# Performance work log

Measured on AMD Instinct MI355X. Metric: run time of the kernel, lower is better.

Reference implementation:

```python
import jax, jax.numpy as jnp
import numpy as np

B, T, C = 4, 2048, 1024
H = 16
HD = C // H  # 64


def setup_inputs() -> dict:
    key = jax.random.key(0)
    ks = jax.random.split(key, 4)
    x = jax.random.normal(ks[0], (B, T, C), dtype=jnp.float32)
    # c_attn: Linear(C, 3C, bias=False)  (qkv_bias=False)
    w_attn = jax.random.normal(ks[1], (C, 3 * C), dtype=jnp.float32) / np.sqrt(C)
    # c_proj: Linear(C, C) with bias (nn.Linear default)
    w_proj = jax.random.normal(ks[2], (C, C), dtype=jnp.float32) / np.sqrt(C)
    b_proj = jax.random.normal(ks[3], (C,), dtype=jnp.float32) * 0.01
    return {"x": x, "w_attn": w_attn, "w_proj": w_proj, "b_proj": b_proj}


def reference(x, w_attn, w_proj, b_proj):
    b, t, c = x.shape
    qkv = x @ w_attn  # [B,T,3C]
    q, k, v = jnp.split(qkv, 3, axis=-1)
    # [B,H,T,HD]
    q = q.reshape(b, t, H, HD).transpose(0, 2, 1, 3)
    k = k.reshape(b, t, H, HD).transpose(0, 2, 1, 3)
    v = v.reshape(b, t, H, HD).transpose(0, 2, 1, 3)
    scale = 1.0 / np.sqrt(HD)
    attn = jnp.einsum('bhqd,bhkd->bhqk', q, k) * scale  # [B,H,T,T]
    causal = jnp.tril(jnp.ones((t, t), dtype=bool))
    attn = jnp.where(causal, attn, -jnp.inf)
    attn = jax.nn.softmax(attn, axis=-1)
    out = jnp.einsum('bhqk,bhkd->bhqd', attn, v)  # [B,H,T,HD]
    out = out.transpose(0, 2, 1, 3).reshape(b, t, c)
    return out @ w_proj + b_proj
```

## Files before the change

### kernel.cpp

```cpp
#include <hip/hip_runtime.h>

#define BB 4
#define TT 2048
#define CC 1024
#define C3 3072
#define HH 16
#define HD 64
#define BT 8192

#define TS 40
#define TSZ (64 * TS)

typedef __bf16 bf16x8 __attribute__((ext_vector_type(8)));
typedef float floatx4 __attribute__((ext_vector_type(4)));
typedef unsigned short u16;

__device__ __forceinline__ u16 f2bf(float f) {
  union { float f; unsigned u; } a; a.f = f;
  return (u16)((a.u + 0x7fffu + ((a.u >> 16) & 1u)) >> 16);
}
__device__ __forceinline__ bf16x8 ld8(const u16* p) { return *(const bf16x8*)p; }
__device__ __forceinline__ floatx4 mfma16(bf16x8 a, bf16x8 b, floatx4 c) {
  return __builtin_amdgcn_mfma_f32_16x16x32_bf16(a, b, c, 0, 0, 0);
}

__global__ __launch_bounds__(256) void tobf16_kernel(const float4* __restrict__ src,
                                                     ushort4* __restrict__ dst, int n4) {
  int i = blockIdx.x * 256 + threadIdx.x;
  if (i >= n4) return;
  float4 v = src[i];
  ushort4 o; o.x = f2bf(v.x); o.y = f2bf(v.y); o.z = f2bf(v.z); o.w = f2bf(v.w);
  dst[i] = o;
}

__global__ __launch_bounds__(256) void transpose_bf16_kernel(const float* __restrict__ src,
                                                             u16* __restrict__ dst,
                                                             int K, int N) {
  __shared__ float s[64][65];
  const int t = threadIdx.x;
  const int r = t >> 4;
  const int c = (t & 15) * 4;
  const int k0 = blockIdx.y * 64, n0 = blockIdx.x * 64;
#pragma unroll
  for (int i = 0; i < 4; ++i) {
    float4 v = *(const float4*)&src[(size_t)(k0 + r + i * 16) * N + n0 + c];
    s[r + i * 16][c + 0] = v.x; s[r + i * 16][c + 1] = v.y;
    s[r + i * 16][c + 2] = v.z; s[r + i * 16][c + 3] = v.w;
  }
  __syncthreads();
#pragma unroll
  for (int i = 0; i < 4; ++i) {
    const int nn = r + i * 16;
    ushort4 o;
    o.x = f2bf(s[c + 0][nn]); o.y = f2bf(s[c + 1][nn]);
    o.z = f2bf(s[c + 2][nn]); o.w = f2bf(s[c + 3][nn]);
    *(ushort4*)&dst[(size_t)(n0 + nn) * K + k0 + c] = o;
  }
}

template<int MODE>
__global__ __launch_bounds__(256) void gemm_kernel(
    const u16* __restrict__ A, const u16* __restrict__ B,
    const float* __restrict__ bias, float* __restrict__ outf,
    u16* __restrict__ qk, u16* __restrict__ vT,
    int M, int N, int K) {
  __shared__ u16 smem[2][2][2 * TSZ];

  const int t = threadIdx.x;
  const int w = t >> 6, lane = t & 63, lr = lane & 15, qd = lane >> 4;
  const int wm = w >> 1, wn = w & 1;
  const int m0 = blockIdx.y * 128, n0 = blockIdx.x * 128;

  const int sr = t >> 2;
  const int sc = (t & 3) * 8;
  const int so = sr * TS + sc;
  const u16* Ag = A + (size_t)(m0 + sr) * K + sc;
  const u16* Bg = B + (size_t)(n0 + sr) * K + sc;

  floatx4 acc[4][4] = {};

  uint4 rA0, rA1, rB0, rB1;
  rA0 = *(const uint4*)(Ag);
  rA1 = *(const uint4*)(Ag + (size_t)64 * K);
  rB0 = *(const uint4*)(Bg);
  rB1 = *(const uint4*)(Bg + (size_t)64 * K);

  for (int k0 = 0; k0 < K; k0 += 32) {
    const int p = (k0 >> 5) & 1;
    u16* sA = &smem[p][0][0];
    u16* sB = &smem[p][1][0];
    *(uint4*)&sA[so]       = rA0;
    *(uint4*)&sA[TSZ + so] = rA1;
    *(uint4*)&sB[so]       = rB0;
    *(uint4*)&sB[TSZ + so] = rB1;
    __syncthreads();
    if (k0 + 32 < K) {
      rA0 = *(const uint4*)(Ag + k0 + 32);
      rA1 = *(const uint4*)(Ag + (size_t)64 * K + k0 + 32);
      rB0 = *(const uint4*)(Bg + k0 + 32);
      rB1 = *(const uint4*)(Bg + (size_t)64 * K + k0 + 32);
    }

    bf16x8 af[4], bf[4];
#pragma unroll
    for (int mj = 0; mj < 4; ++mj) af[mj] = ld8(&sA[(wm * 64 + mj * 16 + lr) * TS + qd * 8]);
#pragma unroll
    for (int nj = 0; nj < 4; ++nj) bf[nj] = ld8(&sB[(wn * 64 + nj * 16 + lr) * TS + qd * 8]);
#pragma unroll
    for (int mj = 0; mj < 4; ++mj)
#pragma unroll
      for (int nj = 0; nj < 4; ++nj)
        acc[mj][nj] = mfma16(af[mj], bf[nj], acc[mj][nj]);
  }

  const int rowg0 = m0 + wm * 64;
  const int colg0 = n0 + wn * 64;
  if constexpr (MODE == 2) {
#pragma unroll
    for (int nj = 0; nj < 4; ++nj) {
      const int col = colg0 + nj * 16 + lr;
      const float bv = bias[col];
#pragma unroll
      for (int mj = 0; mj < 4; ++mj)
#pragma unroll
        for (int i = 0; i < 4; ++i)
          outf[(size_t)(rowg0 + mj * 16 + qd * 4 + i) * N + col] = acc[mj][nj][i] + bv;
    }
  } else {
    __syncthreads();
    u16* Tw = &smem[0][0][0] + w * (32 * 72);
    const bool isV = (n0 >= 2 * CC);
    if (!isV) {
#pragma unroll
      for (int half = 0; half < 2; ++half) {
#pragma unroll
        for (int m2 = 0; m2 < 2; ++m2)
#pragma unroll
          for (int nj = 0; nj < 4; ++nj)
#pragma unroll
            for (int i = 0; i < 4; ++i)
              Tw[(m2 * 16 + qd * 4 + i) * 72 + nj * 16 + lr] =
                  f2bf(acc[half * 2 + m2][nj][i]);
#pragma unroll
        for (int s = 0; s < 4; ++s) {
          const int rl = s * 8 + (lane >> 3);
          const int c0 = (lane & 7) * 8;
          *(bf16x8*)&qk[(size_t)(rowg0 + half * 32 + rl) * (2 * CC) + colg0 + c0] =
              ld8(&Tw[rl * 72 + c0]);
        }
      }
    } else {
      const int bI = m0 >> 11;
      const int tbase = (m0 & (TT - 1)) + wm * 64;
      const int dim0 = colg0 - 2 * CC;
#pragma unroll
      for (int half = 0; half < 2; ++half) {
#pragma unroll
        for (int n2 = 0; n2 < 2; ++n2)
#pragma unroll
          for (int mj = 0; mj < 4; ++mj)
#pragma unroll
            for (int i = 0; i < 4; ++i)
              Tw[(n2 * 16 + lr) * 72 + mj * 16 + qd * 4 + i] =
                  f2bf(acc[mj][half * 2 + n2][i]);
#pragma unroll
        for (int s = 0; s < 4; ++s) {
          const int dl = s * 8 + (lane >> 3);
          const int t0 = (lane & 7) * 8;
          *(bf16x8*)&vT[((size_t)(bI << 10) + dim0 + half * 32 + dl) * TT + tbase + t0] =
              ld8(&Tw[dl * 72 + t0]);
        }
      }
    }
  }
}

__global__ __launch_bounds__(256, 3) void attn_kernel(const u16* __restrict__ qk,
                                                      const u16* __restrict__ vT,
                                                      u16* __restrict__ att) {
  __shared__ u16 sKV[2][4][TSZ];
  __shared__ u16 sP[4 * 16 * 72];

  const int t = threadIdx.x;
  const int w = t >> 6, lane = t & 63, lr = lane & 15, qd = lane >> 4;
  const int qtile = 31 - blockIdx.y;
  const int bh = blockIdx.x;
  const int b = bh >> 4, h = bh & 15;
  const int q0 = qtile * 64;
  const u16* qbase = qk + (size_t)b * TT * (2 * CC);

  const u16* qp = qbase + (size_t)(q0 + w * 16 + lr) * (2 * CC) + h * HD;
  const bf16x8 qf0 = ld8(qp + qd * 8);
  const bf16x8 qf1 = ld8(qp + 32 + qd * 8);

  const int sr = t >> 2, sc = (t & 3) * 8;
  const int so = sr * TS + sc;
  const u16* Kg = qbase + (size_t)sr * (2 * CC) + CC + h * HD + sc;
  const u16* Vg = vT + ((size_t)bh * HD + sr) * TT + sc;

  float lsum = 0.f;
  floatx4 o[4] = {};
  const float SC = 0.125f * 1.44269504089f;
  u16* Pw = &sP[w * 16 * 72];
  const int myq = q0 + w * 16 + lr;

  uint4 rK0, rK1, rV0, rV1;
  rK0 = *(const uint4*)(Kg);
  rK1 = *(const uint4*)(Kg + 32);
  rV0 = *(const uint4*)(Vg);
  rV1 = *(const uint4*)(Vg + 32);

  for (int kt = 0; kt <= qtile; ++kt) {
    u16* base = &sKV[kt & 1][0][0];
    *(uint4*)&base[so]           = rK0;
    *(uint4*)&base[TSZ + so]     = rK1;
    *(uint4*)&base[2 * TSZ + so] = rV0;
    *(uint4*)&base[3 * TSZ + so] = rV1;
    __syncthreads();
    if (kt < qtile) {
      const int kn = (kt + 1) * 64;
      rK0 = *(const uint4*)(Kg + (size_t)kn * (2 * CC));
      rK1 = *(const uint4*)(Kg + (size_t)kn * (2 * CC) + 32);
      rV0 = *(const uint4*)(Vg + kn);
      rV1 = *(const uint4*)(Vg + kn + 32);
    }

    const u16* sK0 = &sKV[kt & 1][0][0];
    const u16* sK1 = &sKV[kt & 1][1][0];
    const u16* sV0 = &sKV[kt & 1][2][0];
    const u16* sV1 = &sKV[kt & 1][3][0];

    floatx4 s[4] = {};
#pragma unroll
    for (int j = 0; j < 4; ++j) {
      bf16x8 kf0 = ld8(&sK0[(j * 16 + lr) * TS + qd * 8]);
      bf16x8 kf1 = ld8(&sK1[(j * 16 + lr) * TS + qd * 8]);
      s[j] = mfma16(kf0, qf0, s[j]);
      s[j] = mfma16(kf1, qf1, s[j]);
    }

    const bool diag = (kt == qtile);
#pragma unroll
    for (int j = 0; j < 4; ++j) {
      float p[4];
#pragma unroll
      for (int i = 0; i < 4; ++i) {
        p[i] = exp2f(s[j][i] * SC);
        if (diag) {
          const int key = kt * 64 + j * 16 + qd * 4 + i;
          p[i] = (key <= myq) ? p[i] : 0.f;
        }
        lsum += p[i];
      }
      uint2 pk;
      pk.x = __builtin_amdgcn_perm(__float_as_uint(p[1]), __float_as_uint(p[0]), 0x07060302);
      pk.y = __builtin_amdgcn_perm(__float_as_uint(p[3]), __float_as_uint(p[2]), 0x07060302);
      *(uint2*)&Pw[lr * 72 + j * 16 + qd * 4] = pk;
    }

    const bf16x8 pf0 = ld8(&Pw[lr * 72 + qd * 8]);
    const bf16x8 pf1 = ld8(&Pw[lr * 72 + 32 + qd * 8]);

#pragma unroll
    for (int j = 0; j < 4; ++j) {
      bf16x8 vf0 = ld8(&sV0[(j * 16 + lr) * TS + qd * 8]);
      bf16x8 vf1 = ld8(&sV1[(j * 16 + lr) * TS + qd * 8]);
      o[j] = mfma16(pf0, vf0, o[j]);
      o[j] = mfma16(pf1, vf1, o[j]);
    }
  }

  lsum += __shfl_xor(lsum, 16);
  lsum += __shfl_xor(lsum, 32);
  float linv[4];
#pragma unroll
  for (int i = 0; i < 4; ++i) linv[i] = 1.0f / __shfl(lsum, qd * 4 + i);

#pragma unroll
  for (int j = 0; j < 4; ++j)
#pragma unroll
    for (int i = 0; i < 4; ++i) {
      const size_t row = (size_t)b * TT + q0 + w * 16 + qd * 4 + i;
      att[row * CC + h * HD + j * 16 + lr] = f2bf(o[j][i] * linv[i]);
    }
}

extern "C" void kernel_launch(void* const* d_in, const int* in_sizes, int n_in,
                              void* d_out, int out_size, void* d_ws, size_t ws_size,
                              hipStream_t stream) {
  const float* x      = (const float*)d_in[0];
  const float* w_attn = (const float*)d_in[1];
  const float* w_proj = (const float*)d_in[2];
  const float* b_proj = (const float*)d_in[3];
  float* out = (float*)d_out;

  char* ws = (char*)d_ws;
  u16* xb  = (u16*)(ws + 0);
  u16* waT = (u16*)(ws + 16777216);
  u16* wpT = (u16*)(ws + 23068672);
  u16* qk  = (u16*)(ws + 25165824);
  u16* vT  = (u16*)(ws + 58720256);
  u16* att = (u16*)(ws + 75497472);

  tobf16_kernel<<<8192, 256, 0, stream>>>((const float4*)x, (ushort4*)xb, 2097152);
  transpose_bf16_kernel<<<dim3(48, 16), 256, 0, stream>>>(w_attn, waT, CC, C3);
  transpose_bf16_kernel<<<dim3(16, 16), 256, 0, stream>>>(w_proj, wpT, CC, CC);

  gemm_kernel<1><<<dim3(24, 64), 256, 0, stream>>>(xb, waT, nullptr, nullptr, qk, vT,
                                                   BT, C3, CC);
  attn_kernel<<<dim3(64, 32), 256, 0, stream>>>(qk, vT, att);

  gemm_kernel<2><<<dim3(8, 64), 256, 0, stream>>>(att, wpT, b_proj, out, nullptr, nullptr,
                                                  BT, CC, CC);
}
```

Baseline: 258.6 us.

## Move softmax P redistribution to permlane swaps and fold scale into Q

The attention kernel no longer stages probabilities through shared memory. It rearranges them across lanes with permlane32/permlane16 swaps, removing the sP buffer and its LDS round-trip. The softmax scale and log2e factor are folded into Q when the QKV GEMM writes it out, so the kernel can use the raw exp2 builtin. The K/V tile stride drops from 40 to 32, which removes padding and may add LDS bank conflicts, and launch bounds rise to 5 blocks per CU for higher occupancy. Correctness depends on the lane-permutation mapping matching the MFMA operand layout.

```diff
diff --git a/kernel.cpp b/kernel.cpp
--- a/kernel.cpp
+++ b/kernel.cpp
@@ -8,11 +8,12 @@
 #define HD 64
 #define BT 8192
 
-#define TS 40
+#define TS 32
 #define TSZ (64 * TS)
 
 typedef __bf16 bf16x8 __attribute__((ext_vector_type(8)));
 typedef float floatx4 __attribute__((ext_vector_type(4)));
+typedef unsigned uintx2 __attribute__((ext_vector_type(2)));
 typedef unsigned short u16;
 
 __device__ __forceinline__ u16 f2bf(float f) {
@@ -22,6 +23,13 @@
 __device__ __forceinline__ bf16x8 ld8(const u16* p) { return *(const bf16x8*)p; }
 __device__ __forceinline__ floatx4 mfma16(bf16x8 a, bf16x8 b, floatx4 c) {
   return __builtin_amdgcn_mfma_f32_16x16x32_bf16(a, b, c, 0, 0, 0);
+}
+
+__device__ __forceinline__ void qd_xchg(unsigned a, unsigned b,
+                                        unsigned& r0, unsigned& r1) {
+  uintx2 t = __builtin_amdgcn_permlane32_swap(a, b, false, false);
+  uintx2 r = __builtin_amdgcn_permlane16_swap(t[0], t[1], false, false);
+  r0 = r[0]; r1 = r[1];
 }
 
 __global__ __launch_bounds__(256) void tobf16_kernel(const float4* __restrict__ src,
@@ -131,6 +139,7 @@
     u16* Tw = &smem[0][0][0] + w * (32 * 72);
     const bool isV = (n0 >= 2 * CC);
     if (!isV) {
+      const float qs = (n0 < CC) ? 0.18033688011f : 1.0f;
 #pragma unroll
       for (int half = 0; half < 2; ++half) {
 #pragma unroll
@@ -140,7 +149,7 @@
 #pragma unroll
             for (int i = 0; i < 4; ++i)
               Tw[(m2 * 16 + qd * 4 + i) * 72 + nj * 16 + lr] =
-                  f2bf(acc[half * 2 + m2][nj][i]);
+                  f2bf(acc[half * 2 + m2][nj][i] * qs);
 #pragma unroll
         for (int s = 0; s < 4; ++s) {
           const int rl = s * 8 + (lane >> 3);
@@ -175,11 +184,10 @@
   }
 }
 
-__global__ __launch_bounds__(256, 3) void attn_kernel(const u16* __restrict__ qk,
+__global__ __launch_bounds__(256, 5) void attn_kernel(const u16* __restrict__ qk,
                                                       const u16* __restrict__ vT,
                                                       u16* __restrict__ att) {
   __shared__ u16 sKV[2][4][TSZ];
-  __shared__ u16 sP[4 * 16 * 72];
 
   const int t = threadIdx.x;
   const int w = t >> 6, lane = t & 63, lr = lane & 15, qd = lane >> 4;
@@ -200,8 +208,6 @@
 
   float lsum = 0.f;
   floatx4 o[4] = {};
-  const float SC = 0.125f * 1.44269504089f;
-  u16* Pw = &sP[w * 16 * 72];
   const int myq = q0 + w * 16 + lr;
 
   uint4 rK0, rK1, rV0, rV1;
@@ -240,26 +246,30 @@
     }
 
     const bool diag = (kt == qtile);
+    unsigned W[4][2];
 #pragma unroll
     for (int j = 0; j < 4; ++j) {
       float p[4];
 #pragma unroll
       for (int i = 0; i < 4; ++i) {
-        p[i] = exp2f(s[j][i] * SC);
+        p[i] = __builtin_amdgcn_exp2f(s[j][i]);
         if (diag) {
           const int key = kt * 64 + j * 16 + qd * 4 + i;
           p[i] = (key <= myq) ? p[i] : 0.f;
         }
         lsum += p[i];
       }
-      uint2 pk;
-      pk.x = __builtin_amdgcn_perm(__float_as_uint(p[1]), __float_as_uint(p[0]), 0x07060302);
-      pk.y = __builtin_amdgcn_perm(__float_as_uint(p[3]), __float_as_uint(p[2]), 0x07060302);
-      *(uint2*)&Pw[lr * 72 + j * 16 + qd * 4] = pk;
-    }
-
-    const bf16x8 pf0 = ld8(&Pw[lr * 72 + qd * 8]);
-    const bf16x8 pf1 = ld8(&Pw[lr * 72 + 32 + qd * 8]);
+      W[j][0] = __builtin_amdgcn_perm(__float_as_uint(p[1]), __float_as_uint(p[0]), 0x07060302);
+      W[j][1] = __builtin_amdgcn_perm(__float_as_uint(p[3]), __float_as_uint(p[2]), 0x07060302);
+    }
+
+    uint4 F0, F1;
+    qd_xchg(W[0][0], W[1][0], F0.x, F0.z);
+    qd_xchg(W[0][1], W[1][1], F0.y, F0.w);
+    qd_xchg(W[2][0], W[3][0], F1.x, F1.z);
+    qd_xchg(W[2][1], W[3][1], F1.y, F1.w);
+    const bf16x8 pf0 = __builtin_bit_cast(bf16x8, F0);
+    const bf16x8 pf1 = __builtin_bit_cast(bf16x8, F1);
 
 #pragma unroll
     for (int j = 0; j < 4; ++j) {
```

Result: faster. 243.1 us (-6.0%).
